# Kernel tuning notes

Hardware: AMD Instinct MI355X
Metric: run time of the kernel (lower is better)

Reference implementation:

```python
import jax, jax.numpy as jnp
import numpy as np

B, S, D, H, E, K = 2, 1024, 1024, 2048, 8, 2


def setup_inputs() -> dict:
    key = jax.random.key(0)
    k1, k2, k3, k4 = jax.random.split(key, 4)
    x = jax.random.normal(k1, (B, S, D), dtype=jnp.float32)
    # router initialized to zeros in the module; use small random weights so
    # top-k routing is non-degenerate for a correctness baseline
    router_w = 0.02 * jax.random.normal(k2, (E, D), dtype=jnp.float32)
    router_b = jnp.zeros((E,), dtype=jnp.float32)
    w12 = 0.02 * jax.random.normal(k3, (E, D, 2 * H), dtype=jnp.float32)
    w3 = 0.02 * jax.random.normal(k4, (E, H, D), dtype=jnp.float32)
    return {"x": x, "router_w": router_w, "router_b": router_b, "w12": w12, "w3": w3}


def reference(x, router_w, router_b, w12, w3):
    # Router (eval mode: no jitter noise)
    logits = jnp.einsum("bsd,ed->bse", x, router_w) + router_b      # [B,S,E]
    scores = jax.nn.sigmoid(logits)
    top_vals, top_idx = jax.lax.top_k(scores, K)                     # [B,S,K]
    rweights = top_vals / (jnp.sum(top_vals, axis=-1, keepdims=True) + 1e-6)
    # per-expert combine weight: sum over top-k slots where idx == e
    onehot = jax.nn.one_hot(top_idx, E, dtype=x.dtype)               # [B,S,K,E]
    combine = jnp.einsum("bsk,bske->bse", rweights, onehot)          # [B,S,E]
    # Dense per-expert SwiGLU over all tokens (matches naive module math)
    h12 = jnp.einsum("bsd,edh->ebsh", x, w12)                        # [E,B,S,2H]
    h1, h2 = jnp.split(h12, 2, axis=-1)
    hidden = jax.nn.silu(h1) * h2                                    # [E,B,S,H]
    expert_out = jnp.einsum("ebsh,ehd->ebsd", hidden, w3)            # [E,B,S,D]
    out = jnp.einsum("ebsd,bse->bsd", expert_out, combine)           # [B,S,D]
    aux_loss = 0.01 * jnp.mean(logits ** 2)
    return out, aux_loss
```

## Files before the change

kernel.cpp:

```cpp
#include <hip/hip_runtime.h>
#include <math.h>
#include <stdint.h>

#define B_ 2
#define S_ 1024
#define D_ 1024
#define H_ 2048
#define E_ 8
#define TOK_ (B_*S_)
#define N1_ (2*H_)
#define PAIRS_ (TOK_*2)
#define MAXTILES_ 40

typedef float f32x4 __attribute__((ext_vector_type(4)));
typedef short short8 __attribute__((ext_vector_type(8)));

__device__ __forceinline__ unsigned short f2bf(float f) {
  unsigned int u = __float_as_uint(f);
  u += 0x7fffu + ((u >> 16) & 1u);
  return (unsigned short)(u >> 16);
}

__global__ __launch_bounds__(256) void transpose_f32_to_bf16(
    const float* __restrict__ src, unsigned short* __restrict__ dst, int R, int C)
{
  __shared__ float tile[64][65];
  const int e = blockIdx.z;
  const float* s = src + (size_t)e * R * C;
  unsigned short* d = dst + (size_t)e * R * C;
  const int c0 = blockIdx.x * 64, r0 = blockIdx.y * 64;
  const int tx = threadIdx.x & 63;
  const int ty = threadIdx.x >> 6;
#pragma unroll
  for (int i = 0; i < 16; ++i) {
    int r = ty + i * 4;
    tile[r][tx] = s[(size_t)(r0 + r) * C + c0 + tx];
  }
  __syncthreads();
  const int rx = (threadIdx.x & 31) * 2;
  const int cy = threadIdx.x >> 5;
#pragma unroll
  for (int i = 0; i < 8; ++i) {
    int c = cy + i * 8;
    ushort2 o;
    o.x = f2bf(tile[rx][c]);
    o.y = f2bf(tile[rx + 1][c]);
    *(ushort2*)&d[(size_t)(c0 + c) * R + r0 + rx] = o;
  }
}

__global__ __launch_bounds__(256) void router_kernel(
    const float* __restrict__ x, const float* __restrict__ rw,
    const float* __restrict__ rb, int* __restrict__ counts,
    int* __restrict__ expert_of, int* __restrict__ slot_of,
    float* __restrict__ w_of, float* __restrict__ tok_ssq)
{
  const int wave = threadIdx.x >> 6, lane = threadIdx.x & 63;
  const int t = blockIdx.x * 4 + wave;
  const float4* x4 = (const float4*)(x + (size_t)t * D_);
  const float4* rw4 = (const float4*)rw;
  float acc[E_];
#pragma unroll
  for (int e = 0; e < E_; ++e) acc[e] = 0.f;
#pragma unroll
  for (int d4 = 0; d4 < D_ / 4 / 64; ++d4) {
    int idx = d4 * 64 + lane;
    float4 xv = x4[idx];
#pragma unroll
    for (int e = 0; e < E_; ++e) {
      float4 wv = rw4[e * (D_ / 4) + idx];
      acc[e] += xv.x * wv.x + xv.y * wv.y + xv.z * wv.z + xv.w * wv.w;
    }
  }
#pragma unroll
  for (int e = 0; e < E_; ++e) {
    float v = acc[e];
#pragma unroll
    for (int sh = 32; sh > 0; sh >>= 1) v += __shfl_xor(v, sh, 64);
    acc[e] = v;
  }
  if (lane == 0) {
    float logits[E_], sc[E_], ssq = 0.f;
#pragma unroll
    for (int e = 0; e < E_; ++e) {
      logits[e] = acc[e] + rb[e];
      ssq += logits[e] * logits[e];
      sc[e] = 1.f / (1.f + __expf(-logits[e]));
    }
    tok_ssq[t] = ssq;
    int i1 = 0;
#pragma unroll
    for (int e = 1; e < E_; ++e) if (sc[e] > sc[i1]) i1 = e;
    int i2 = (i1 == 0) ? 1 : 0;
#pragma unroll
    for (int e = 0; e < E_; ++e)
      if (e != i1 && e != i2 && sc[e] > sc[i2]) i2 = e;
    float v1 = sc[i1], v2 = sc[i2];
    float inv = 1.f / (v1 + v2 + 1e-6f);
    int s1 = atomicAdd(&counts[i1], 1);
    int s2 = atomicAdd(&counts[i2], 1);
    expert_of[t * 2]     = i1; slot_of[t * 2]     = s1; w_of[t * 2]     = v1 * inv;
    expert_of[t * 2 + 1] = i2; slot_of[t * 2 + 1] = s2; w_of[t * 2 + 1] = v2 * inv;
  }
}

__global__ void offsets_kernel(const int* __restrict__ counts, int* __restrict__ offsets,
                               int* __restrict__ tile_e, int* __restrict__ tile_m0)
{
  if (threadIdx.x == 0) {
    int o = 0, nt = 0;
    for (int e = 0; e < E_; ++e) {
      offsets[e] = o;
      for (int m0 = 0; m0 < counts[e]; m0 += 128) {
        tile_e[nt] = e; tile_m0[nt] = m0; ++nt;
      }
      o += counts[e];
    }
    for (; nt < MAXTILES_; ++nt) tile_e[nt] = -1;
  }
}

__global__ __launch_bounds__(256) void aux_kernel(const float* __restrict__ tok_ssq,
                                                  float* __restrict__ out_aux)
{
  __shared__ float sm[256];
  float s = 0.f;
  for (int i = threadIdx.x; i < TOK_; i += 256) s += tok_ssq[i];
  sm[threadIdx.x] = s;
  __syncthreads();
  for (int h = 128; h > 0; h >>= 1) {
    if (threadIdx.x < h) sm[threadIdx.x] += sm[threadIdx.x + h];
    __syncthreads();
  }
  if (threadIdx.x == 0) *out_aux = 0.01f * sm[0] / (float)(TOK_ * E_);
}

__global__ __launch_bounds__(256) void pack_kernel(
    const float* __restrict__ x, const int* __restrict__ expert_of,
    const int* __restrict__ slot_of, const float* __restrict__ w_of,
    const int* __restrict__ offsets, unsigned short* __restrict__ px,
    int* __restrict__ tok_ids, float* __restrict__ tok_w)
{
  const int pair = blockIdx.x;
  const int t = pair >> 1;
  const int e = expert_of[pair];
  const int row = offsets[e] + slot_of[pair];
  if (threadIdx.x == 0) { tok_ids[row] = t; tok_w[row] = w_of[pair]; }
  const float4* xr = (const float4*)(x + (size_t)t * D_);
  ushort4* pr = (ushort4*)(px + (size_t)row * D_);
  float4 v = xr[threadIdx.x];
  ushort4 o;
  o.x = f2bf(v.x); o.y = f2bf(v.y); o.z = f2bf(v.z); o.w = f2bf(v.w);
  pr[threadIdx.x] = o;
}

__device__ __forceinline__ void stage_tile(const unsigned short* gbase, int gstride,
                                           unsigned short* sbase, int kk,
                                           int wave, int lane)
{
  const int seg = (lane & 3) ^ ((lane >> 3) & 3);
#pragma unroll
  for (int c = 0; c < 2; ++c) {
    const unsigned short* g = gbase
        + (size_t)(wave * 32 + c * 16 + (lane >> 2)) * gstride + kk + seg * 8;
    unsigned short* s = sbase + (wave * 32 + c * 16) * 32;
    __builtin_amdgcn_global_load_lds(
        (const __attribute__((address_space(1))) void*)g,
        (__attribute__((address_space(3))) void*)s, 16, 0, 0);
  }
}

__device__ __forceinline__ void stage_tile_clamped(const unsigned short* gbase, int gstride,
                                                   int row0, int rowmax,
                                                   unsigned short* sbase, int kk,
                                                   int wave, int lane)
{
  const int seg = (lane & 3) ^ ((lane >> 3) & 3);
#pragma unroll
  for (int c = 0; c < 2; ++c) {
    int r = row0 + wave * 32 + c * 16 + (lane >> 2);
    r = (r < rowmax) ? r : rowmax - 1;
    const unsigned short* g = gbase + (size_t)r * gstride + kk + seg * 8;
    unsigned short* s = sbase + (wave * 32 + c * 16) * 32;
    __builtin_amdgcn_global_load_lds(
        (const __attribute__((address_space(1))) void*)g,
        (__attribute__((address_space(3))) void*)s, 16, 0, 0);
  }
}

__device__ __forceinline__ short8 read_frag(const unsigned short* smem, int row, int lk) {
  const int s = lk ^ ((row >> 1) & 3);
  return *(const short8*)&smem[row * 32 + s * 8];
}

__global__ __launch_bounds__(256, 2) void gemm1_kernel(
    const unsigned short* __restrict__ px, const unsigned short* __restrict__ w12t,
    unsigned short* __restrict__ hid, const int* __restrict__ counts,
    const int* __restrict__ offsets, const int* __restrict__ tile_e,
    const int* __restrict__ tile_m0)
{
  const int ti = blockIdx.y, nt = blockIdx.x;
  const int e = tile_e[ti];
  if (e < 0) return;
  const int m0 = tile_m0[ti];
  const int cnt = counts[e];
  const int off = offsets[e];
  const int tid = threadIdx.x;
  const int wave = tid >> 6, lane = tid & 63;
  const int wm = wave >> 1, wn = wave & 1;
  const int lr = lane & 15, lk = lane >> 4;

  __shared__ __align__(16) unsigned short As[128 * 32];
  __shared__ __align__(16) unsigned short B1s[128 * 32];
  __shared__ __align__(16) unsigned short B2s[128 * 32];

  f32x4 zero = {0.f, 0.f, 0.f, 0.f};
  f32x4 acc1[4][4], acc2[4][4];
#pragma unroll
  for (int mi = 0; mi < 4; ++mi)
#pragma unroll
    for (int ni = 0; ni < 4; ++ni) { acc1[mi][ni] = zero; acc2[mi][ni] = zero; }

  const unsigned short* B1base = w12t + ((size_t)e * N1_ + nt * 128) * D_;
  const unsigned short* B2base = w12t + ((size_t)e * N1_ + H_ + nt * 128) * D_;

  for (int kk = 0; kk < D_; kk += 32) {
    stage_tile_clamped(px, D_, off + m0, PAIRS_, As, kk, wave, lane);
    stage_tile(B1base, D_, B1s, kk, wave, lane);
    stage_tile(B2base, D_, B2s, kk, wave, lane);
    __syncthreads();
    short8 a[4], b1[4], b2[4];
#pragma unroll
    for (int i = 0; i < 4; ++i) {
      a[i]  = read_frag(As,  wm * 64 + i * 16 + lr, lk);
      b1[i] = read_frag(B1s, wn * 64 + i * 16 + lr, lk);
      b2[i] = read_frag(B2s, wn * 64 + i * 16 + lr, lk);
    }
#pragma unroll
    for (int mi = 0; mi < 4; ++mi)
#pragma unroll
      for (int ni = 0; ni < 4; ++ni) {
        acc1[mi][ni] = __builtin_amdgcn_mfma_f32_16x16x32_bf16(a[mi], b1[ni], acc1[mi][ni], 0, 0, 0);
        acc2[mi][ni] = __builtin_amdgcn_mfma_f32_16x16x32_bf16(a[mi], b2[ni], acc2[mi][ni], 0, 0, 0);
      }
    __syncthreads();
  }

#pragma unroll
  for (int mi = 0; mi < 4; ++mi)
#pragma unroll
    for (int r = 0; r < 4; ++r) {
      int row_local = m0 + wm * 64 + mi * 16 + lk * 4 + r;
      if (row_local < cnt) {
#pragma unroll
        for (int ni = 0; ni < 4; ++ni) {
          int col = nt * 128 + wn * 64 + ni * 16 + lr;
          float v1 = acc1[mi][ni][r];
          float v2 = acc2[mi][ni][r];
          float hval = (v1 / (1.f + __expf(-v1))) * v2;
          hid[(size_t)(off + row_local) * H_ + col] = f2bf(hval);
        }
      }
    }
}

__global__ __launch_bounds__(256, 4) void gemm2_kernel(
    const unsigned short* __restrict__ hid, const unsigned short* __restrict__ w3t,
    const int* __restrict__ counts, const int* __restrict__ offsets,
    const int* __restrict__ tile_e, const int* __restrict__ tile_m0,
    const int* __restrict__ tok_ids, const float* __restrict__ tok_w,
    float* __restrict__ out)
{
  const int ti = blockIdx.y, nt = blockIdx.x, ks = blockIdx.z;
  const int e = tile_e[ti];
  if (e < 0) return;
  const int m0 = tile_m0[ti];
  const int cnt = counts[e];
  const int off = offsets[e];
  const int tid = threadIdx.x;
  const int wave = tid >> 6, lane = tid & 63;
  const int wm = wave >> 1, wn = wave & 1;
  const int lr = lane & 15, lk = lane >> 4;

  __shared__ __align__(16) unsigned short As[128 * 32];
  __shared__ __align__(16) unsigned short Bs[128 * 32];

  f32x4 zero = {0.f, 0.f, 0.f, 0.f};
  f32x4 acc[4][4];
#pragma unroll
  for (int mi = 0; mi < 4; ++mi)
#pragma unroll
    for (int ni = 0; ni < 4; ++ni) acc[mi][ni] = zero;

  const unsigned short* Bbase = w3t + ((size_t)e * D_ + nt * 128) * H_;

  const int k0 = ks * (H_ / 2), k1 = k0 + (H_ / 2);
  for (int kk = k0; kk < k1; kk += 32) {
    stage_tile_clamped(hid, H_, off + m0, PAIRS_, As, kk, wave, lane);
    stage_tile(Bbase, H_, Bs, kk, wave, lane);
    __syncthreads();
    short8 a[4], b[4];
#pragma unroll
    for (int i = 0; i < 4; ++i) {
      a[i] = read_frag(As, wm * 64 + i * 16 + lr, lk);
      b[i] = read_frag(Bs, wn * 64 + i * 16 + lr, lk);
    }
#pragma unroll
    for (int mi = 0; mi < 4; ++mi)
#pragma unroll
      for (int ni = 0; ni < 4; ++ni)
        acc[mi][ni] = __builtin_amdgcn_mfma_f32_16x16x32_bf16(a[mi], b[ni], acc[mi][ni], 0, 0, 0);
    __syncthreads();
  }

#pragma unroll
  for (int mi = 0; mi < 4; ++mi)
#pragma unroll
    for (int r = 0; r < 4; ++r) {
      int row_local = m0 + wm * 64 + mi * 16 + lk * 4 + r;
      if (row_local < cnt) {
        int g = off + row_local;
        int t = tok_ids[g];
        float wgt = tok_w[g];
#pragma unroll
        for (int ni = 0; ni < 4; ++ni) {
          int col = nt * 128 + wn * 64 + ni * 16 + lr;
          atomicAdd(&out[(size_t)t * D_ + col], acc[mi][ni][r] * wgt);
        }
      }
    }
}

extern "C" void kernel_launch(void* const* d_in, const int* in_sizes, int n_in,
                              void* d_out, int out_size, void* d_ws, size_t ws_size,
                              hipStream_t stream)
{
  const float* x   = (const float*)d_in[0];
  const float* rw  = (const float*)d_in[1];
  const float* rb  = (const float*)d_in[2];
  const float* w12 = (const float*)d_in[3];
  const float* w3  = (const float*)d_in[4];
  float* out = (float*)d_out;

  char* wsb = (char*)d_ws;
  int*   counts    = (int*)(wsb + 0);
  int*   offsets   = (int*)(wsb + 64);
  int*   tile_e    = (int*)(wsb + 128);
  int*   tile_m0   = (int*)(wsb + 384);
  int*   expert_of = (int*)(wsb + 1024);
  int*   slot_of   = (int*)(wsb + 1024 + 16384);
  float* w_of      = (float*)(wsb + 1024 + 2 * 16384);
  int*   tok_ids   = (int*)(wsb + 1024 + 3 * 16384);
  float* tok_w     = (float*)(wsb + 1024 + 4 * 16384);
  float* tok_ssq   = (float*)(wsb + 1024 + 5 * 16384);
  unsigned short* px   = (unsigned short*)(wsb + (128 << 10));
  unsigned short* hid  = (unsigned short*)(wsb + (128 << 10) + ((size_t)8  << 20));
  unsigned short* w12t = (unsigned short*)(wsb + (128 << 10) + ((size_t)24 << 20));
  unsigned short* w3t  = (unsigned short*)(wsb + (128 << 10) + ((size_t)88 << 20));

  hipMemsetAsync(counts, 0, E_ * sizeof(int), stream);
  hipMemsetAsync(out, 0, (size_t)out_size * sizeof(float), stream);

  transpose_f32_to_bf16<<<dim3(N1_ / 64, D_ / 64, E_), 256, 0, stream>>>(w12, w12t, D_, N1_);
  transpose_f32_to_bf16<<<dim3(D_ / 64, H_ / 64, E_), 256, 0, stream>>>(w3, w3t, H_, D_);
  router_kernel<<<TOK_ / 4, 256, 0, stream>>>(x, rw, rb, counts, expert_of, slot_of, w_of, tok_ssq);
  offsets_kernel<<<1, 64, 0, stream>>>(counts, offsets, tile_e, tile_m0);
  aux_kernel<<<1, 256, 0, stream>>>(tok_ssq, out + (size_t)TOK_ * D_);
  pack_kernel<<<PAIRS_, 256, 0, stream>>>(x, expert_of, slot_of, w_of, offsets, px, tok_ids, tok_w);
  gemm1_kernel<<<dim3(16, MAXTILES_), 256, 0, stream>>>(px, w12t, hid, counts, offsets, tile_e, tile_m0);
  gemm2_kernel<<<dim3(8, MAXTILES_, 2), 256, 0, stream>>>(hid, w3t, counts, offsets, tile_e, tile_m0, tok_ids, tok_w, out);
}
```

Before: 445.7 us.

## Replace atomic scatter-add in down-projection with per-split buffers and a gather combine

The down-projection GEMM now writes plain fp32 partial results per k-split into a workspace buffer instead of atomically adding weighted values into the output. A new combine kernel gathers each token's two expert rows from both k-splits and applies the routing weights. The output memset is dropped, and the offsets and aux-loss kernels are merged into one launch. This removes atomic contention and the memset, at the cost of an extra write and read of about 32 MB of intermediates plus one more launch.

After: 431.0 us. 3.3% less time.

```diff
diff --git a/kernel.cpp b/kernel.cpp
--- a/kernel.cpp
+++ b/kernel.cpp
@@ -104,8 +104,10 @@
   }
 }
 
-__global__ void offsets_kernel(const int* __restrict__ counts, int* __restrict__ offsets,
-                               int* __restrict__ tile_e, int* __restrict__ tile_m0)
+__global__ __launch_bounds__(256) void meta_kernel(
+    const int* __restrict__ counts, const float* __restrict__ tok_ssq,
+    int* __restrict__ offsets, int* __restrict__ tile_e, int* __restrict__ tile_m0,
+    float* __restrict__ out_aux)
 {
   if (threadIdx.x == 0) {
     int o = 0, nt = 0;
@@ -118,11 +120,6 @@
     }
     for (; nt < MAXTILES_; ++nt) tile_e[nt] = -1;
   }
-}
-
-__global__ __launch_bounds__(256) void aux_kernel(const float* __restrict__ tok_ssq,
-                                                  float* __restrict__ out_aux)
-{
   __shared__ float sm[256];
   float s = 0.f;
   for (int i = threadIdx.x; i < TOK_; i += 256) s += tok_ssq[i];
@@ -137,15 +134,14 @@
 
 __global__ __launch_bounds__(256) void pack_kernel(
     const float* __restrict__ x, const int* __restrict__ expert_of,
-    const int* __restrict__ slot_of, const float* __restrict__ w_of,
-    const int* __restrict__ offsets, unsigned short* __restrict__ px,
-    int* __restrict__ tok_ids, float* __restrict__ tok_w)
+    const int* __restrict__ slot_of, const int* __restrict__ offsets,
+    unsigned short* __restrict__ px, int* __restrict__ pair_row)
 {
   const int pair = blockIdx.x;
   const int t = pair >> 1;
   const int e = expert_of[pair];
   const int row = offsets[e] + slot_of[pair];
-  if (threadIdx.x == 0) { tok_ids[row] = t; tok_w[row] = w_of[pair]; }
+  if (threadIdx.x == 0) pair_row[pair] = row;
   const float4* xr = (const float4*)(x + (size_t)t * D_);
   ushort4* pr = (ushort4*)(px + (size_t)row * D_);
   float4 v = xr[threadIdx.x];
@@ -268,8 +264,7 @@
     const unsigned short* __restrict__ hid, const unsigned short* __restrict__ w3t,
     const int* __restrict__ counts, const int* __restrict__ offsets,
     const int* __restrict__ tile_e, const int* __restrict__ tile_m0,
-    const int* __restrict__ tok_ids, const float* __restrict__ tok_w,
-    float* __restrict__ out)
+    float* __restrict__ ybuf)
 {
   const int ti = blockIdx.y, nt = blockIdx.x, ks = blockIdx.z;
   const int e = tile_e[ti];
@@ -293,6 +288,7 @@
     for (int ni = 0; ni < 4; ++ni) acc[mi][ni] = zero;
 
   const unsigned short* Bbase = w3t + ((size_t)e * D_ + nt * 128) * H_;
+  float* yb = ybuf + (size_t)ks * PAIRS_ * D_;
 
   const int k0 = ks * (H_ / 2), k1 = k0 + (H_ / 2);
   for (int kk = k0; kk < k1; kk += 32) {
@@ -320,15 +316,35 @@
       int row_local = m0 + wm * 64 + mi * 16 + lk * 4 + r;
       if (row_local < cnt) {
         int g = off + row_local;
-        int t = tok_ids[g];
-        float wgt = tok_w[g];
 #pragma unroll
         for (int ni = 0; ni < 4; ++ni) {
           int col = nt * 128 + wn * 64 + ni * 16 + lr;
-          atomicAdd(&out[(size_t)t * D_ + col], acc[mi][ni][r] * wgt);
+          yb[(size_t)g * D_ + col] = acc[mi][ni][r];
         }
       }
     }
+}
+
+__global__ __launch_bounds__(256) void combine_kernel(
+    const float* __restrict__ ybuf, const int* __restrict__ pair_row,
+    const float* __restrict__ w_of, float* __restrict__ out)
+{
+  const int t = blockIdx.x;
+  const int r0 = pair_row[t * 2], r1 = pair_row[t * 2 + 1];
+  const float w0 = w_of[t * 2], w1 = w_of[t * 2 + 1];
+  const float4* y0 = (const float4*)(ybuf);
+  const float4* y1 = (const float4*)(ybuf + (size_t)PAIRS_ * D_);
+  const int i = threadIdx.x;
+  float4 a0 = y0[(size_t)r0 * (D_ / 4) + i];
+  float4 b0 = y1[(size_t)r0 * (D_ / 4) + i];
+  float4 a1 = y0[(size_t)r1 * (D_ / 4) + i];
+  float4 b1 = y1[(size_t)r1 * (D_ / 4) + i];
+  float4 o;
+  o.x = w0 * (a0.x + b0.x) + w1 * (a1.x + b1.x);
+  o.y = w0 * (a0.y + b0.y) + w1 * (a1.y + b1.y);
+  o.z = w0 * (a0.z + b0.z) + w1 * (a1.z + b1.z);
+  o.w = w0 * (a0.w + b0.w) + w1 * (a1.w + b1.w);
+  ((float4*)out)[(size_t)t * (D_ / 4) + i] = o;
 }
 
 extern "C" void kernel_launch(void* const* d_in, const int* in_sizes, int n_in,
@@ -350,23 +366,22 @@
   int*   expert_of = (int*)(wsb + 1024);
   int*   slot_of   = (int*)(wsb + 1024 + 16384);
   float* w_of      = (float*)(wsb + 1024 + 2 * 16384);
-  int*   tok_ids   = (int*)(wsb + 1024 + 3 * 16384);
-  float* tok_w     = (float*)(wsb + 1024 + 4 * 16384);
-  float* tok_ssq   = (float*)(wsb + 1024 + 5 * 16384);
+  int*   pair_row  = (int*)(wsb + 1024 + 3 * 16384);
+  float* tok_ssq   = (float*)(wsb + 1024 + 4 * 16384);
   unsigned short* px   = (unsigned short*)(wsb + (128 << 10));
   unsigned short* hid  = (unsigned short*)(wsb + (128 << 10) + ((size_t)8  << 20));
   unsigned short* w12t = (unsigned short*)(wsb + (128 << 10) + ((size_t)24 << 20));
   unsigned short* w3t  = (unsigned short*)(wsb + (128 << 10) + ((size_t)88 << 20));
+  float*          ybuf = (float*)(wsb + (128 << 10) + ((size_t)120 << 20));
 
   hipMemsetAsync(counts, 0, E_ * sizeof(int), stream);
-  hipMemsetAsync(out, 0, (size_t)out_size * sizeof(float), stream);
 
   transpose_f32_to_bf16<<<dim3(N1_ / 64, D_ / 64, E_), 256, 0, stream>>>(w12, w12t, D_, N1_);
   transpose_f32_to_bf16<<<dim3(D_ / 64, H_ / 64, E_), 256, 0, stream>>>(w3, w3t, H_, D_);
   router_kernel<<<TOK_ / 4, 256, 0, stream>>>(x, rw, rb, counts, expert_of, slot_of, w_of, tok_ssq);
-  offsets_kernel<<<1, 64, 0, stream>>>(counts, offsets, tile_e, tile_m0);
-  aux_kernel<<<1, 256, 0, stream>>>(tok_ssq, out + (size_t)TOK_ * D_);
-  pack_kernel<<<PAIRS_, 256, 0, stream>>>(x, expert_of, slot_of, w_of, offsets, px, tok_ids, tok_w);
+  meta_kernel<<<1, 256, 0, stream>>>(counts, tok_ssq, offsets, tile_e, tile_m0, out + (size_t)TOK_ * D_);
+  pack_kernel<<<PAIRS_, 256, 0, stream>>>(x, expert_of, slot_of, offsets, px, pair_row);
   gemm1_kernel<<<dim3(16, MAXTILES_), 256, 0, stream>>>(px, w12t, hid, counts, offsets, tile_e, tile_m0);
-  gemm2_kernel<<<dim3(8, MAXTILES_, 2), 256, 0, stream>>>(hid, w3t, counts, offsets, tile_e, tile_m0, tok_ids, tok_w, out);
-}
+  gemm2_kernel<<<dim3(8, MAXTILES_, 2), 256, 0, stream>>>(hid, w3t, counts, offsets, tile_e, tile_m0, ybuf);
+  combine_kernel<<<TOK_, 256, 0, stream>>>(ybuf, pair_row, w_of, out);
+}
```
